# Kernel optimization log

Measured on AMD Instinct MI355X. Metric: run time of the kernel, lower is better.

The kernel has to match this reference:

```python
import jax, jax.numpy as jnp
import numpy as np

NUM_CLASS = 20
STRIDE = 4.0
B, H, W, G, NV = 8, 128, 128, 64, 40


def setup_inputs() -> dict:
    key = jax.random.key(0)
    ks = jax.random.split(key, 8)
    keypoints = jax.random.normal(ks[0], (B, H, W, NUM_CLASS), jnp.float32)
    preg = jax.random.uniform(ks[1], (B, H, W, 4), jnp.float32, 1.0, 40.0)
    fpn = jax.random.normal(ks[2], (B, H, W, NUM_CLASS), jnp.float32)
    masks = jnp.ones((B, H, W, G), jnp.float32)
    scalar_y = jax.random.uniform(ks[3], (B, G), jnp.float32, 5.0, 25.0)
    scalar_x = jax.random.uniform(ks[4], (B, G), jnp.float32, 5.0, 25.0)
    # ground truth: [cy, cx, y1, x1, y2, x2, class]; rows >= NV are zero padding
    rng = np.random.default_rng(0)
    gt = np.zeros((B, G, 7), np.float32)
    cy = rng.uniform(20.0, 492.0, (B, NV)).astype(np.float32)
    cx = rng.uniform(20.0, 492.0, (B, NV)).astype(np.float32)
    hh = rng.uniform(16.0, 120.0, (B, NV)).astype(np.float32)
    ww = rng.uniform(16.0, 120.0, (B, NV)).astype(np.float32)
    gt[:, :NV, 0] = cy
    gt[:, :NV, 1] = cx
    gt[:, :NV, 2] = np.clip(cy - hh / 2, 1.0, 510.0)
    gt[:, :NV, 3] = np.clip(cx - ww / 2, 1.0, 510.0)
    gt[:, :NV, 4] = np.clip(cy + hh / 2, 1.0, 510.0)
    gt[:, :NV, 5] = np.clip(cx + ww / 2, 1.0, 510.0)
    gt[:, :NV, 6] = rng.integers(1, NUM_CLASS + 1, (B, NV)).astype(np.float32)
    return {
        "keypoints": keypoints,
        "preg": preg,
        "fpn": fpn,
        "ground_truth": jnp.asarray(gt),
        "masks": masks,
        "scalar_y": scalar_y,
        "scalar_x": scalar_x,
    }


def _image_loss(gravity_pred, dist_pred, heatmap_pred, gt, masks, sy, sx):
    f32 = jnp.float32
    Hh, Ww, C = gravity_pred.shape
    Gg = gt.shape[0]
    # padding boundary: first row whose cy (col 0) is the minimum (==0 padding)
    slice_index = jnp.argmin(gt[:, 0])
    valid = jnp.arange(Gg) < slice_index
    vf = valid.astype(f32)

    gy = (gt[:, 0] + 0.5) / STRIDE
    gx = (gt[:, 1] + 0.5) / STRIDE
    by1 = (gt[:, 2] + 0.5) / STRIDE
    bx1 = (gt[:, 3] + 0.5) / STRIDE
    by2 = (gt[:, 4] + 0.5) / STRIDE
    bx2 = (gt[:, 5] + 0.5) / STRIDE
    cid = gt[:, 6].astype(jnp.int32) - 1
    kp_y = jnp.clip(jnp.floor(gt[:, 0] / STRIDE).astype(jnp.int32), 0, Hh - 1)
    kp_x = jnp.clip(jnp.floor(gt[:, 1] / STRIDE).astype(jnp.int32), 0, Ww - 1)

    grid_y = (jnp.arange(Hh, dtype=f32) + 0.5)[:, None, None]  # [H,1,1]
    grid_x = (jnp.arange(Ww, dtype=f32) + 0.5)[None, :, None]  # [1,W,1]

    dist_l = grid_x - bx1  # [1,W,G]
    dist_r = bx2 - grid_x
    dist_t = grid_y - by1  # [H,1,G]
    dist_b = by2 - grid_y
    ymask = (dist_t > 0.0).astype(f32) * (dist_b > 0.0).astype(f32)
    xmask = (dist_l > 0.0).astype(f32) * (dist_r > 0.0).astype(f32)
    heatmask = ymask * xmask * masks * vf  # [H,W,G]
    dist_l = dist_l * heatmask
    dist_r = dist_r * heatmask
    dist_t = dist_t * heatmask
    dist_b = dist_b * heatmask
    loc = jnp.max(heatmask, axis=-1)  # [H,W]
    dist_area = (dist_l + dist_r) * (dist_t + dist_b)
    area_pad = dist_area + (1.0 - heatmask) * 1e8
    area_min = jnp.min(area_pad, axis=-1, keepdims=True)
    dist_mask = (dist_area == area_min).astype(f32) * loc[..., None]  # [H,W,G]
    dl = jnp.max(dist_l * dist_mask, axis=-1)
    dr = jnp.max(dist_r * dist_mask, axis=-1)
    dt = jnp.max(dist_t * dist_mask, axis=-1)
    db = jnp.max(dist_b * dist_mask, axis=-1)

    pl, pr, pt, pb = (dist_pred[..., k] for k in range(4))
    inter = (jnp.minimum(dl, pl) + jnp.minimum(dr, pr)) * (jnp.minimum(dt, pt) + jnp.minimum(db, pb))
    union = (dl + dr) * (dt + db) + (pl + pr) * (pt + pb) - inter
    iou = inter / (union + 1e-12)

    red = jnp.exp(-(((grid_y - 0.5 - jnp.floor(gy)) / jnp.sqrt(sy)) ** 2
                    + ((grid_x - 0.5 - jnp.floor(gx)) / jnp.sqrt(sx)) ** 2) / 2.0) * vf  # [H,W,G]
    iou_red = jnp.max(red, axis=-1)
    iou_loss = jnp.sum(-jnp.log(iou + 1e-12) * loc * (iou_red * 4.0 + 1.0))

    # per-class max over gts of that class (== boolean_mask + reduce_max; empty -> 0)
    seg = jnp.where(valid & (cid >= 0) & (cid < C), cid, C)
    red_gt = jnp.maximum(jax.ops.segment_max(red.transpose(2, 0, 1), seg, num_segments=C + 1)[:C], 0.0).transpose(1, 2, 0)
    hm_gt = jnp.maximum(jax.ops.segment_max(dist_mask.transpose(2, 0, 1), seg, num_segments=C + 1)[:C], 0.0).transpose(1, 2, 0)
    gt_kp = jnp.zeros((Hh, Ww, C + 1), f32).at[kp_y, kp_x, seg].max(vf)[..., :C]

    sig, ls = jax.nn.sigmoid, jax.nn.log_sigmoid
    pos = -(1.0 - sig(gravity_pred)) ** 2 * ls(gravity_pred) * gt_kp
    neg = -(1.0 - red_gt) ** 4 * sig(gravity_pred) ** 2 * (-gravity_pred + ls(gravity_pred)) * (1.0 - gt_kp)
    gravity_loss = jnp.sum(pos) + jnp.sum(neg)

    hpos = -10.0 * (1.0 - sig(heatmap_pred)) ** 2 * ls(heatmap_pred) * hm_gt
    hneg = -10.0 * sig(heatmap_pred) ** 2 * (-heatmap_pred + ls(heatmap_pred)) * (1.0 - hm_gt)
    s_hg = jnp.sum(hm_gt)
    hm_loss = jnp.sum(hneg) / (jnp.asarray(Hh * Ww * C, f32) - s_hg)

    cond = s_hg != 0.0
    safe_hg = jnp.where(cond, s_hg, 1.0)
    s_loc = jnp.sum(loc)
    safe_loc = jnp.where(s_loc > 0.0, s_loc, 1.0)
    n_valid = jnp.maximum(slice_index.astype(f32), 1.0)
    hm2 = hm_loss + jnp.sum(hpos) / safe_hg
    iou_out = jnp.where(cond, iou_loss / safe_loc, 0.0)
    grav_out = jnp.where(cond, gravity_loss / n_valid, 0.0)
    hm_out = jnp.where(cond, hm2, hm_loss)
    total = jnp.where(cond, iou_out + grav_out + hm2, hm_loss)
    return iou_out, hm_out, grav_out, total


def reference(keypoints, preg, fpn, ground_truth, masks, scalar_y, scalar_x):
    losses = jax.vmap(_image_loss)(keypoints, preg, fpn, ground_truth, masks, scalar_y, scalar_x)
    # layer returns the mean total loss over the batch
    return jnp.mean(losses[3])
```

## Files before the change

kernel.cpp:

```cpp
#include <hip/hip_runtime.h>
#include <math.h>

#define Bc 8
#define Hc 128
#define Wc 128
#define Cc 20
#define Gc 64
#define HWc (Hc*Wc)

#define WS_STRIDE 768
#define WS_NV   704
#define WS_ACC  705
#define WS_SLICE 711

__global__ __launch_bounds__(64) void prep_kernel(
    const float* __restrict__ gt, const float* __restrict__ sy,
    const float* __restrict__ sx, float* __restrict__ ws)
{
  const int b = blockIdx.x;
  const int g = threadIdx.x;
  __shared__ float cy_s[Gc];
  __shared__ int slice_s;
  const float* row = gt + (size_t)(b*Gc + g)*7;
  const float cy = row[0];
  const float cx = row[1];
  cy_s[g] = cy;
  __syncthreads();
  if (g == 0) {
    float mn = cy_s[0]; int idx = 0;
    for (int i = 1; i < Gc; ++i) { float v = cy_s[i]; if (v < mn) { mn = v; idx = i; } }
    slice_s = idx;
  }
  __syncthreads();
  const int slice = slice_s;
  float* wb = ws + (size_t)b*WS_STRIDE;
  int*  wbi = (int*)wb;
  wb[0*Gc+g] = (row[2]+0.5f)*0.25f;
  wb[1*Gc+g] = (row[3]+0.5f)*0.25f;
  wb[2*Gc+g] = (row[4]+0.5f)*0.25f;
  wb[3*Gc+g] = (row[5]+0.5f)*0.25f;
  wb[4*Gc+g] = floorf((cy+0.5f)*0.25f);
  wb[5*Gc+g] = floorf((cx+0.5f)*0.25f);
  wb[6*Gc+g] = 1.0f / sy[b*Gc+g];
  wb[7*Gc+g] = 1.0f / sx[b*Gc+g];
  const float vf = (g < slice) ? 1.0f : 0.0f;
  wb[8*Gc+g] = vf;
  const int cid = (int)row[6] - 1;
  wbi[9*Gc+g] = (vf > 0.0f && cid >= 0 && cid < Cc) ? cid : Cc;
  int kpy = (int)floorf(cy*0.25f); kpy = kpy < 0 ? 0 : (kpy > Hc-1 ? Hc-1 : kpy);
  int kpx = (int)floorf(cx*0.25f); kpx = kpx < 0 ? 0 : (kpx > Wc-1 ? Wc-1 : kpx);
  wbi[10*Gc+g] = kpy*Wc + kpx;
  if (g == 0) { wb[WS_NV] = fmaxf((float)slice, 1.0f); wbi[WS_SLICE] = slice; }
  if (g < 6) wb[WS_ACC+g] = 0.0f;
}

__device__ __forceinline__ float logsig(float x) {
  return fminf(x, 0.0f) - log1pf(__expf(-fabsf(x)));
}
__device__ __forceinline__ float sigmoidf_(float x) {
  return 1.0f / (1.0f + __expf(-x));
}
__device__ __forceinline__ float wave_sum(float v) {
  #pragma unroll
  for (int o = 32; o > 0; o >>= 1) v += __shfl_down(v, o, 64);
  return v;
}

__global__ __launch_bounds__(256) void main_kernel(
  const float* __restrict__ kpt, const float* __restrict__ preg,
  const float* __restrict__ fpn, const float* __restrict__ masks,
  float* __restrict__ ws)
{
  __shared__ float s_pg[704];
  __shared__ float s_rmax[256*21];
  __shared__ float s_part[4][6];

  const int tid = threadIdx.x;
  const int b   = blockIdx.x >> 6;
  const int pix = blockIdx.x*256 + tid;
  const int hw  = pix & (HWc-1);
  const int h = hw >> 7, w = hw & (Wc-1);

  float* wb = ws + (size_t)b*WS_STRIDE;
  { const int* src = (const int*)wb; int* dst = (int*)s_pg;
    for (int i = tid; i < 704; i += 256) dst[i] = src[i]; }
  float* rme = s_rmax + tid*21;
  #pragma unroll
  for (int c = 0; c < 21; ++c) rme[c] = 0.0f;
  __syncthreads();

  const float* s_by1 = s_pg;
  const float* s_bx1 = s_pg + 64;
  const float* s_by2 = s_pg + 128;
  const float* s_bx2 = s_pg + 192;
  const float* s_fgy = s_pg + 256;
  const float* s_fgx = s_pg + 320;
  const float* s_isy = s_pg + 384;
  const float* s_isx = s_pg + 448;
  const int*   s_seg = (const int*)(s_pg + 576);
  const int*   s_kpx = (const int*)(s_pg + 640);
  const int nslice = ((const int*)wb)[WS_SLICE];

  const float wx = w + 0.5f, hy = h + 0.5f;
  const float px_ = (float)w, py_ = (float)h;
  const float* mrow = masks + (size_t)pix * Gc;

  float amin = 3.0e38f; int gmin = -1;
  float loc = 0.0f, iou_red = 0.0f;
  unsigned kpmask = 0;

  for (int g0 = 0; g0 < nslice; g0 += 4) {
    const float4 m4 = *(const float4*)(mrow + g0);
    #pragma unroll
    for (int j = 0; j < 4; ++j) {
      const int g = g0 + j;
      if (g >= nslice) break;
      const float m = (j==0) ? m4.x : (j==1) ? m4.y : (j==2) ? m4.z : m4.w;
      const float dl = wx - s_bx1[g], dr = s_bx2[g] - wx;
      const float dt = hy - s_by1[g], db = s_by2[g] - hy;
      const bool inbox = (dl > 0.0f) & (dr > 0.0f) & (dt > 0.0f) & (db > 0.0f);
      const float hm = inbox ? m : 0.0f;
      const float area = (dl*hm + dr*hm) * (dt*hm + db*hm);
      const float ap = area + (1.0f - hm)*1e8f;
      if (ap < amin) { amin = ap; gmin = g; }
      loc = fmaxf(loc, hm);
      const float dy = py_ - s_fgy[g], dx = px_ - s_fgx[g];
      const float red = __expf(-0.5f*(dy*dy*s_isy[g] + dx*dx*s_isx[g]));
      iou_red = fmaxf(iou_red, red);
      const int c = s_seg[g];
      if (c < Cc) {
        if (red > rme[c]) rme[c] = red;
        if (s_kpx[g] == hw) kpmask |= (1u << c);
      }
    }
  }

  float dlm=0.0f, drm=0.0f, dtm=0.0f, dbm=0.0f; int cmin = Cc; float hmval = 0.0f;
  if (loc > 0.0f && gmin >= 0) {
    const float m = mrow[gmin];
    const float dl = wx - s_bx1[gmin], dr = s_bx2[gmin] - wx;
    const float dt = hy - s_by1[gmin], db = s_by2[gmin] - hy;
    dlm = dl*m*loc; drm = dr*m*loc; dtm = dt*m*loc; dbm = db*m*loc;
    cmin = s_seg[gmin];
    hmval = loc;
  }

  const float4 p4 = *(const float4*)(preg + (size_t)pix*4);
  const float inter = (fminf(dlm,p4.x)+fminf(drm,p4.y)) * (fminf(dtm,p4.z)+fminf(dbm,p4.w));
  const float uni = (dlm+drm)*(dtm+dbm) + (p4.x+p4.y)*(p4.z+p4.w) - inter;
  const float iou = inter / (uni + 1e-12f);
  const float t_iou = -logf(iou + 1e-12f) * loc * (iou_red*4.0f + 1.0f);

  float grav = 0.0f, hpos = 0.0f, hneg = 0.0f, shg = 0.0f;
  const float* kq = kpt + (size_t)pix*Cc;
  const float* fq = fpn + (size_t)pix*Cc;
  #pragma unroll
  for (int c = 0; c < Cc; ++c) {
    const float x   = kq[c];
    const float s   = sigmoidf_(x);
    const float lsx = logsig(x);
    const float rmax = rme[c];
    const float kpv  = ((kpmask >> c) & 1u) ? 1.0f : 0.0f;
    const float om  = 1.0f - rmax;
    const float om4 = (om*om)*(om*om);
    const float oms = 1.0f - s;
    const float pos_t = -(oms*oms)*lsx;
    const float neg_t = -om4*(s*s)*(lsx - x);
    grav += pos_t*kpv + neg_t*(1.0f - kpv);

    const float fx  = fq[c];
    const float sf  = sigmoidf_(fx);
    const float lsf = logsig(fx);
    const float hg  = (c == cmin) ? hmval : 0.0f;
    const float osf = 1.0f - sf;
    hpos += -10.0f*(osf*osf)*lsf*hg;
    hneg += -10.0f*(sf*sf)*(lsf - fx)*(1.0f - hg);
    shg  += hg;
  }

  float v0 = wave_sum(t_iou);
  float v1 = wave_sum(loc);
  float v2 = wave_sum(grav);
  float v3 = wave_sum(hpos);
  float v4 = wave_sum(hneg);
  float v5 = wave_sum(shg);
  const int wv = tid >> 6, ln = tid & 63;
  if (ln == 0) {
    s_part[wv][0]=v0; s_part[wv][1]=v1; s_part[wv][2]=v2;
    s_part[wv][3]=v3; s_part[wv][4]=v4; s_part[wv][5]=v5;
  }
  __syncthreads();
  if (tid < 6) {
    const float a = s_part[0][tid] + s_part[1][tid] + s_part[2][tid] + s_part[3][tid];
    atomicAdd(wb + WS_ACC + tid, a);
  }
}

__global__ __launch_bounds__(64) void fin_kernel(const float* __restrict__ ws,
                                                 float* __restrict__ out)
{
  const int b = threadIdx.x;
  float total = 0.0f;
  if (b < Bc) {
    const float* wb = ws + (size_t)b*WS_STRIDE;
    const float iou_loss = wb[WS_ACC+0];
    const float s_loc    = wb[WS_ACC+1];
    const float grav     = wb[WS_ACC+2];
    const float hposs    = wb[WS_ACC+3];
    const float hnegs    = wb[WS_ACC+4];
    const float shg      = wb[WS_ACC+5];
    const float nv       = wb[WS_NV];
    const float hm_loss  = hnegs / ((float)(HWc*Cc) - shg);
    const bool  cond     = (shg != 0.0f);
    const float safe_hg  = cond ? shg : 1.0f;
    const float safe_loc = (s_loc > 0.0f) ? s_loc : 1.0f;
    const float hm2      = hm_loss + hposs/safe_hg;
    total = cond ? (iou_loss/safe_loc + grav/nv + hm2) : hm_loss;
  }
  #pragma unroll
  for (int o = 4; o > 0; o >>= 1) total += __shfl_down(total, o, 64);
  if (b == 0) out[0] = total * (1.0f/(float)Bc);
}

extern "C" void kernel_launch(void* const* d_in, const int* in_sizes, int n_in,
                              void* d_out, int out_size, void* d_ws, size_t ws_size,
                              hipStream_t stream) {
  const float* kpt  = (const float*)d_in[0];
  const float* preg = (const float*)d_in[1];
  const float* fpn  = (const float*)d_in[2];
  const float* gt   = (const float*)d_in[3];
  const float* mk   = (const float*)d_in[4];
  const float* sy   = (const float*)d_in[5];
  const float* sx   = (const float*)d_in[6];
  float* ws  = (float*)d_ws;
  float* out = (float*)d_out;

  prep_kernel<<<Bc, 64, 0, stream>>>(gt, sy, sx, ws);
  main_kernel<<<(Bc*HWc)/256, 256, 0, stream>>>(kpt, preg, fpn, mk, ws);
  fin_kernel<<<1, 64, 0, stream>>>(ws, out);
}
```

Baseline: 127.9 us.

## Bucket ground-truth by class, drop per-thread LDS max array, fuse final reduction

The prep kernel now sorts valid ground-truth entries into per-class buckets. The main kernel computes each class's gaussian max in registers while looping over classes, instead of keeping a 21-float per-thread max array in shared memory. The heatmap positive term is evaluated only for the matched class rather than masked across all 20 classes, and log1pf/logf are replaced with fast intrinsics. The finish kernel is removed and replaced by a last-block-done atomic counter inside the main kernel. These changes cut shared memory pressure, which should raise occupancy, and remove one launch, at the cost of extra prep work, a serial tail in the last block, and an added area==amin check that could change which box is matched.

```diff
diff --git a/kernel.cpp b/kernel.cpp
--- a/kernel.cpp
+++ b/kernel.cpp
@@ -7,11 +7,24 @@
 #define Cc 20
 #define Gc 64
 #define HWc (Hc*Wc)
+#define NBLK (Bc*HWc/256)
 
 #define WS_STRIDE 768
-#define WS_NV   704
-#define WS_ACC  705
-#define WS_SLICE 711
+#define OFF_BY1   0
+#define OFF_BX1   64
+#define OFF_BY2   128
+#define OFF_BX2   192
+#define OFF_FGY   256
+#define OFF_FGX   320
+#define OFF_ISY   384
+#define OFF_ISX   448
+#define OFF_KPIX  512
+#define OFF_SEG   576
+#define OFF_START 640
+#define WS_NV     704
+#define WS_ACC    705
+#define WS_SLICE  712
+#define WS_CNT    713
 
 __global__ __launch_bounds__(64) void prep_kernel(
     const float* __restrict__ gt, const float* __restrict__ sy,
@@ -20,11 +33,13 @@
   const int b = blockIdx.x;
   const int g = threadIdx.x;
   __shared__ float cy_s[Gc];
+  __shared__ int counts[Cc+1], offs[Cc+1], start_s[Cc+2];
   __shared__ int slice_s;
   const float* row = gt + (size_t)(b*Gc + g)*7;
   const float cy = row[0];
   const float cx = row[1];
   cy_s[g] = cy;
+  if (g < Cc+1) { counts[g] = 0; offs[g] = 0; }
   __syncthreads();
   if (g == 0) {
     float mn = cy_s[0]; int idx = 0;
@@ -33,29 +48,43 @@
   }
   __syncthreads();
   const int slice = slice_s;
+  const bool valid = g < slice;
+  const int cid = (int)row[6] - 1;
+  const int cls = (cid >= 0 && cid < Cc) ? cid : Cc;
+  if (valid) atomicAdd(&counts[cls], 1);
+  __syncthreads();
+  if (g == 0) {
+    int acc = 0;
+    for (int c = 0; c < Cc+1; ++c) { start_s[c] = acc; acc += counts[c]; }
+    start_s[Cc+1] = acc;
+  }
+  __syncthreads();
+
   float* wb = ws + (size_t)b*WS_STRIDE;
   int*  wbi = (int*)wb;
-  wb[0*Gc+g] = (row[2]+0.5f)*0.25f;
-  wb[1*Gc+g] = (row[3]+0.5f)*0.25f;
-  wb[2*Gc+g] = (row[4]+0.5f)*0.25f;
-  wb[3*Gc+g] = (row[5]+0.5f)*0.25f;
-  wb[4*Gc+g] = floorf((cy+0.5f)*0.25f);
-  wb[5*Gc+g] = floorf((cx+0.5f)*0.25f);
-  wb[6*Gc+g] = 1.0f / sy[b*Gc+g];
-  wb[7*Gc+g] = 1.0f / sx[b*Gc+g];
-  const float vf = (g < slice) ? 1.0f : 0.0f;
-  wb[8*Gc+g] = vf;
-  const int cid = (int)row[6] - 1;
-  wbi[9*Gc+g] = (vf > 0.0f && cid >= 0 && cid < Cc) ? cid : Cc;
-  int kpy = (int)floorf(cy*0.25f); kpy = kpy < 0 ? 0 : (kpy > Hc-1 ? Hc-1 : kpy);
-  int kpx = (int)floorf(cx*0.25f); kpx = kpx < 0 ? 0 : (kpx > Wc-1 ? Wc-1 : kpx);
-  wbi[10*Gc+g] = kpy*Wc + kpx;
+  wb[OFF_BY1+g] = (row[2]+0.5f)*0.25f;
+  wb[OFF_BX1+g] = (row[3]+0.5f)*0.25f;
+  wb[OFF_BY2+g] = (row[4]+0.5f)*0.25f;
+  wb[OFF_BX2+g] = (row[5]+0.5f)*0.25f;
+  wbi[OFF_SEG+g] = (valid && cls < Cc) ? cls : Cc;
+  if (valid) {
+    const int pos = start_s[cls] + atomicAdd(&offs[cls], 1);
+    wb[OFF_FGY+pos] = floorf((cy+0.5f)*0.25f);
+    wb[OFF_FGX+pos] = floorf((cx+0.5f)*0.25f);
+    wb[OFF_ISY+pos] = 1.0f / sy[b*Gc+g];
+    wb[OFF_ISX+pos] = 1.0f / sx[b*Gc+g];
+    int kpy = (int)floorf(cy*0.25f); kpy = kpy < 0 ? 0 : (kpy > Hc-1 ? Hc-1 : kpy);
+    int kpx = (int)floorf(cx*0.25f); kpx = kpx < 0 ? 0 : (kpx > Wc-1 ? Wc-1 : kpx);
+    wbi[OFF_KPIX+pos] = kpy*Wc + kpx;
+  }
+  if (g < Cc+2) wbi[OFF_START+g] = start_s[g];
   if (g == 0) { wb[WS_NV] = fmaxf((float)slice, 1.0f); wbi[WS_SLICE] = slice; }
   if (g < 6) wb[WS_ACC+g] = 0.0f;
+  if (b == 0 && g == 0) ((int*)ws)[WS_CNT] = 0;
 }
 
 __device__ __forceinline__ float logsig(float x) {
-  return fminf(x, 0.0f) - log1pf(__expf(-fabsf(x)));
+  return fminf(x, 0.0f) - __logf(1.0f + __expf(-fabsf(x)));
 }
 __device__ __forceinline__ float sigmoidf_(float x) {
   return 1.0f / (1.0f + __expf(-x));
@@ -69,10 +98,9 @@
 __global__ __launch_bounds__(256) void main_kernel(
   const float* __restrict__ kpt, const float* __restrict__ preg,
   const float* __restrict__ fpn, const float* __restrict__ masks,
-  float* __restrict__ ws)
+  float* __restrict__ ws, float* __restrict__ out)
 {
   __shared__ float s_pg[704];
-  __shared__ float s_rmax[256*21];
   __shared__ float s_part[4][6];
 
   const int tid = threadIdx.x;
@@ -84,21 +112,19 @@
   float* wb = ws + (size_t)b*WS_STRIDE;
   { const int* src = (const int*)wb; int* dst = (int*)s_pg;
     for (int i = tid; i < 704; i += 256) dst[i] = src[i]; }
-  float* rme = s_rmax + tid*21;
-  #pragma unroll
-  for (int c = 0; c < 21; ++c) rme[c] = 0.0f;
-  __syncthreads();
-
-  const float* s_by1 = s_pg;
-  const float* s_bx1 = s_pg + 64;
-  const float* s_by2 = s_pg + 128;
-  const float* s_bx2 = s_pg + 192;
-  const float* s_fgy = s_pg + 256;
-  const float* s_fgx = s_pg + 320;
-  const float* s_isy = s_pg + 384;
-  const float* s_isx = s_pg + 448;
-  const int*   s_seg = (const int*)(s_pg + 576);
-  const int*   s_kpx = (const int*)(s_pg + 640);
+  __syncthreads();
+
+  const float* s_by1 = s_pg + OFF_BY1;
+  const float* s_bx1 = s_pg + OFF_BX1;
+  const float* s_by2 = s_pg + OFF_BY2;
+  const float* s_bx2 = s_pg + OFF_BX2;
+  const float* s_fgy = s_pg + OFF_FGY;
+  const float* s_fgx = s_pg + OFF_FGX;
+  const float* s_isy = s_pg + OFF_ISY;
+  const float* s_isx = s_pg + OFF_ISX;
+  const int*   s_kpix = (const int*)(s_pg + OFF_KPIX);
+  const int*   s_seg  = (const int*)(s_pg + OFF_SEG);
+  const int*   s_start= (const int*)(s_pg + OFF_START);
   const int nslice = ((const int*)wb)[WS_SLICE];
 
   const float wx = w + 0.5f, hy = h + 0.5f;
@@ -106,9 +132,7 @@
   const float* mrow = masks + (size_t)pix * Gc;
 
   float amin = 3.0e38f; int gmin = -1;
-  float loc = 0.0f, iou_red = 0.0f;
-  unsigned kpmask = 0;
-
+  float loc = 0.0f;
   for (int g0 = 0; g0 < nslice; g0 += 4) {
     const float4 m4 = *(const float4*)(mrow + g0);
     #pragma unroll
@@ -124,15 +148,39 @@
       const float ap = area + (1.0f - hm)*1e8f;
       if (ap < amin) { amin = ap; gmin = g; }
       loc = fmaxf(loc, hm);
-      const float dy = py_ - s_fgy[g], dx = px_ - s_fgx[g];
-      const float red = __expf(-0.5f*(dy*dy*s_isy[g] + dx*dx*s_isx[g]));
+    }
+  }
+
+  const float* kq = kpt + (size_t)pix*Cc;
+  const float* fq = fpn + (size_t)pix*Cc;
+  float iou_red = 0.0f, grav = 0.0f, hneg = 0.0f;
+  for (int c = 0; c < Cc; ++c) {
+    const int s0 = s_start[c], s1 = s_start[c+1];
+    float rmax = 0.0f; bool kpv = false;
+    for (int i = s0; i < s1; ++i) {
+      const float dy = py_ - s_fgy[i], dx = px_ - s_fgx[i];
+      const float red = __expf(-0.5f*(dy*dy*s_isy[i] + dx*dx*s_isx[i]));
       iou_red = fmaxf(iou_red, red);
-      const int c = s_seg[g];
-      if (c < Cc) {
-        if (red > rme[c]) rme[c] = red;
-        if (s_kpx[g] == hw) kpmask |= (1u << c);
-      }
-    }
+      rmax = fmaxf(rmax, red);
+      kpv = kpv | (s_kpix[i] == hw);
+    }
+    const float x   = kq[c];
+    const float s   = sigmoidf_(x);
+    const float lsx = logsig(x);
+    const float kf  = kpv ? 1.0f : 0.0f;
+    const float om  = 1.0f - rmax;
+    const float om4 = (om*om)*(om*om);
+    const float oms = 1.0f - s;
+    grav += (-(oms*oms)*lsx)*kf + (-om4*(s*s)*(lsx - x))*(1.0f - kf);
+
+    const float fx  = fq[c];
+    const float sf  = sigmoidf_(fx);
+    const float lsf = logsig(fx);
+    hneg += -10.0f*(sf*sf)*(lsf - fx);
+  }
+  for (int i = s_start[Cc]; i < s_start[Cc+1]; ++i) {
+    const float dy = py_ - s_fgy[i], dx = px_ - s_fgx[i];
+    iou_red = fmaxf(iou_red, __expf(-0.5f*(dy*dy*s_isy[i] + dx*dx*s_isx[i])));
   }
 
   float dlm=0.0f, drm=0.0f, dtm=0.0f, dbm=0.0f; int cmin = Cc; float hmval = 0.0f;
@@ -140,42 +188,29 @@
     const float m = mrow[gmin];
     const float dl = wx - s_bx1[gmin], dr = s_bx2[gmin] - wx;
     const float dt = hy - s_by1[gmin], db = s_by2[gmin] - hy;
-    dlm = dl*m*loc; drm = dr*m*loc; dtm = dt*m*loc; dbm = db*m*loc;
-    cmin = s_seg[gmin];
-    hmval = loc;
+    const float area = (dl*m + dr*m) * (dt*m + db*m);
+    if (area == amin) {
+      dlm = dl*m*loc; drm = dr*m*loc; dtm = dt*m*loc; dbm = db*m*loc;
+      cmin = s_seg[gmin];
+      hmval = loc;
+    }
   }
 
   const float4 p4 = *(const float4*)(preg + (size_t)pix*4);
   const float inter = (fminf(dlm,p4.x)+fminf(drm,p4.y)) * (fminf(dtm,p4.z)+fminf(dbm,p4.w));
   const float uni = (dlm+drm)*(dtm+dbm) + (p4.x+p4.y)*(p4.z+p4.w) - inter;
   const float iou = inter / (uni + 1e-12f);
-  const float t_iou = -logf(iou + 1e-12f) * loc * (iou_red*4.0f + 1.0f);
-
-  float grav = 0.0f, hpos = 0.0f, hneg = 0.0f, shg = 0.0f;
-  const float* kq = kpt + (size_t)pix*Cc;
-  const float* fq = fpn + (size_t)pix*Cc;
-  #pragma unroll
-  for (int c = 0; c < Cc; ++c) {
-    const float x   = kq[c];
-    const float s   = sigmoidf_(x);
-    const float lsx = logsig(x);
-    const float rmax = rme[c];
-    const float kpv  = ((kpmask >> c) & 1u) ? 1.0f : 0.0f;
-    const float om  = 1.0f - rmax;
-    const float om4 = (om*om)*(om*om);
-    const float oms = 1.0f - s;
-    const float pos_t = -(oms*oms)*lsx;
-    const float neg_t = -om4*(s*s)*(lsx - x);
-    grav += pos_t*kpv + neg_t*(1.0f - kpv);
-
-    const float fx  = fq[c];
+  const float t_iou = -__logf(iou + 1e-12f) * loc * (iou_red*4.0f + 1.0f);
+
+  float hpos = 0.0f, shg = 0.0f;
+  if (hmval > 0.0f && cmin < Cc) {
+    const float fx  = fq[cmin];
     const float sf  = sigmoidf_(fx);
     const float lsf = logsig(fx);
-    const float hg  = (c == cmin) ? hmval : 0.0f;
     const float osf = 1.0f - sf;
-    hpos += -10.0f*(osf*osf)*lsf*hg;
-    hneg += -10.0f*(sf*sf)*(lsf - fx)*(1.0f - hg);
-    shg  += hg;
+    hpos = -10.0f*(osf*osf)*lsf*hmval;
+    hneg -= (-10.0f*(sf*sf)*(lsf - fx))*hmval;
+    shg = hmval;
   }
 
   float v0 = wave_sum(t_iou);
@@ -194,32 +229,33 @@
     const float a = s_part[0][tid] + s_part[1][tid] + s_part[2][tid] + s_part[3][tid];
     atomicAdd(wb + WS_ACC + tid, a);
   }
-}
-
-__global__ __launch_bounds__(64) void fin_kernel(const float* __restrict__ ws,
-                                                 float* __restrict__ out)
-{
-  const int b = threadIdx.x;
-  float total = 0.0f;
-  if (b < Bc) {
-    const float* wb = ws + (size_t)b*WS_STRIDE;
-    const float iou_loss = wb[WS_ACC+0];
-    const float s_loc    = wb[WS_ACC+1];
-    const float grav     = wb[WS_ACC+2];
-    const float hposs    = wb[WS_ACC+3];
-    const float hnegs    = wb[WS_ACC+4];
-    const float shg      = wb[WS_ACC+5];
-    const float nv       = wb[WS_NV];
-    const float hm_loss  = hnegs / ((float)(HWc*Cc) - shg);
-    const bool  cond     = (shg != 0.0f);
-    const float safe_hg  = cond ? shg : 1.0f;
-    const float safe_loc = (s_loc > 0.0f) ? s_loc : 1.0f;
-    const float hm2      = hm_loss + hposs/safe_hg;
-    total = cond ? (iou_loss/safe_loc + grav/nv + hm2) : hm_loss;
-  }
-  #pragma unroll
-  for (int o = 4; o > 0; o >>= 1) total += __shfl_down(total, o, 64);
-  if (b == 0) out[0] = total * (1.0f/(float)Bc);
+  __syncthreads();
+
+  if (tid == 0) {
+    __threadfence();
+    const int done = atomicAdd(&((int*)ws)[WS_CNT], 1);
+    if (done == NBLK - 1) {
+      __threadfence();
+      float total = 0.0f;
+      for (int bb = 0; bb < Bc; ++bb) {
+        float* ab = ws + (size_t)bb*WS_STRIDE;
+        const float iou_loss = atomicAdd(ab+WS_ACC+0, 0.0f);
+        const float s_loc    = atomicAdd(ab+WS_ACC+1, 0.0f);
+        const float gravs    = atomicAdd(ab+WS_ACC+2, 0.0f);
+        const float hposs    = atomicAdd(ab+WS_ACC+3, 0.0f);
+        const float hnegs    = atomicAdd(ab+WS_ACC+4, 0.0f);
+        const float shgs     = atomicAdd(ab+WS_ACC+5, 0.0f);
+        const float nv       = atomicAdd(ab+WS_NV,    0.0f);
+        const float hm_loss  = hnegs / ((float)(HWc*Cc) - shgs);
+        const bool  cond     = (shgs != 0.0f);
+        const float safe_hg  = cond ? shgs : 1.0f;
+        const float safe_loc = (s_loc > 0.0f) ? s_loc : 1.0f;
+        const float hm2      = hm_loss + hposs/safe_hg;
+        total += cond ? (iou_loss/safe_loc + gravs/nv + hm2) : hm_loss;
+      }
+      out[0] = total * (1.0f/(float)Bc);
+    }
+  }
 }
 
 extern "C" void kernel_launch(void* const* d_in, const int* in_sizes, int n_in,
@@ -236,6 +272,5 @@
   float* out = (float*)d_out;
 
   prep_kernel<<<Bc, 64, 0, stream>>>(gt, sy, sx, ws);
-  main_kernel<<<(Bc*HWc)/256, 256, 0, stream>>>(kpt, preg, fpn, mk, ws);
-  fin_kernel<<<1, 64, 0, stream>>>(ws, out);
-}
+  main_kernel<<<NBLK, 256, 0, stream>>>(kpt, preg, fpn, mk, ws, out);
+}
```

After: 159.8 us. 1.25x slower.
